# Kernel tuning notes

Measured on AMD Instinct MI355X. Metric: run time of the kernel, lower is better.

The kernel has to match this reference:

```python
import jax, jax.numpy as jnp
import numpy as np

B, S, H = 2, 2048, 4096
NH, NKV, HD = 32, 8, 128
ROPE_THETA = 10000.0


def _rope_tables(seq_len, head_dim, theta):
    inv_freq = 1.0 / (theta ** (jnp.arange(0, head_dim, 2, dtype=jnp.float32) / head_dim))
    t = jnp.arange(seq_len, dtype=jnp.float32)
    freqs = jnp.outer(t, inv_freq)            # [S, HD/2]
    emb = jnp.concatenate([freqs, freqs], axis=-1)  # [S, HD]
    return jnp.cos(emb), jnp.sin(emb)


def _rotate_half(x):
    x1, x2 = jnp.split(x, 2, axis=-1)
    return jnp.concatenate([-x2, x1], axis=-1)


def setup_inputs() -> dict:
    key = jax.random.key(0)
    ks = jax.random.split(key, 5)
    hidden_states = jax.random.normal(ks[0], (B, S, H), dtype=jnp.float32)
    # causal additive mask [B,1,S,S]
    neg = jnp.finfo(jnp.float32).min
    causal = jnp.where(jnp.tril(jnp.ones((S, S), dtype=bool)), 0.0, neg)
    attention_mask = jnp.broadcast_to(causal[None, None], (B, 1, S, S)).astype(jnp.float32)
    position_ids = jnp.broadcast_to(jnp.arange(S, dtype=jnp.int64)[None], (B, S))
    scale = 0.02
    Wq = jax.random.normal(ks[1], (H, H), dtype=jnp.float32) * scale
    Wk = jax.random.normal(ks[2], (NKV * HD, H), dtype=jnp.float32) * scale
    Wv = jax.random.normal(ks[3], (NKV * HD, H), dtype=jnp.float32) * scale
    Wo = jax.random.normal(ks[4], (H, H), dtype=jnp.float32) * scale
    return {"hidden_states": hidden_states, "attention_mask": attention_mask,
            "position_ids": position_ids, "Wq": Wq, "Wk": Wk, "Wv": Wv, "Wo": Wo}


def reference(hidden_states, attention_mask, position_ids, Wq, Wk, Wv, Wo):
    bsz, q_len, _ = hidden_states.shape
    # projections (nn.Linear: x @ W.T)
    q = (hidden_states @ Wq.T).reshape(bsz, q_len, NH, HD).transpose(0, 2, 1, 3)    # [B,NH,S,HD]
    k = (hidden_states @ Wk.T).reshape(bsz, q_len, NKV, HD).transpose(0, 2, 1, 3)   # [B,NKV,S,HD]
    v = (hidden_states @ Wv.T).reshape(bsz, q_len, NKV, HD).transpose(0, 2, 1, 3)
    # RoPE
    cos, sin = _rope_tables(q_len, HD, ROPE_THETA)
    cos = cos[position_ids][:, None]   # [B,1,S,HD]
    sin = sin[position_ids][:, None]
    q = q * cos + _rotate_half(q) * sin
    k = k * cos + _rotate_half(k) * sin
    # repeat_kv (GQA): [B,NKV,S,HD] -> [B,NH,S,HD]
    n_rep = NH // NKV
    k = jnp.repeat(k, n_rep, axis=1)
    v = jnp.repeat(v, n_rep, axis=1)
    # attention
    attn = jnp.einsum('bhqd,bhkd->bhqk', q, k) / jnp.sqrt(jnp.float32(HD))
    attn = attn + attention_mask
    attn = jax.nn.softmax(attn.astype(jnp.float32), axis=-1).astype(q.dtype)
    out = jnp.einsum('bhqk,bhkd->bhqd', attn, v)           # [B,NH,S,HD]
    out = out.transpose(0, 2, 1, 3).reshape(bsz, q_len, NH * HD)
    return out @ Wo.T
```

## Files before the change

### kernel.cpp

```cpp
#include <hip/hip_runtime.h>
#include <hip/hip_bf16.h>


typedef __bf16 bf16;
typedef __bf16 bf16x8 __attribute__((ext_vector_type(8)));
typedef float f32x4 __attribute__((ext_vector_type(4)));

#define UNROLL _Pragma("unroll")

__device__ __forceinline__ void async16(const bf16* g, bf16* l) {
  __builtin_amdgcn_global_load_lds(
      (const __attribute__((address_space(1))) void*)g,
      (__attribute__((address_space(3))) void*)l,
      16, 0, 0);
}

#define BARR { __builtin_amdgcn_s_barrier(); }
#define VMCNT(n) { asm volatile("s_waitcnt vmcnt(" #n ")" ::: "memory"); }

__global__ void k_cvt(const float* __restrict__ s, bf16* __restrict__ d, int n8) {
  int i = blockIdx.x * 256 + threadIdx.x;
  if (i >= n8) return;
  const float4* sp = (const float4*)s + (size_t)i * 2;
  float4 a = sp[0], b = sp[1];
  bf16x8 o = { (bf16)a.x, (bf16)a.y, (bf16)a.z, (bf16)a.w,
               (bf16)b.x, (bf16)b.y, (bf16)b.z, (bf16)b.w };
  *(bf16x8*)(d + (size_t)i * 8) = o;
}

__global__ void k_cvt4(const float* __restrict__ Xs, const float* __restrict__ Wq,
                       const float* __restrict__ Wk, const float* __restrict__ Wv,
                       bf16* __restrict__ Xb, bf16* __restrict__ Wqkv) {
  int u = blockIdx.x * 256 + threadIdx.x;
  const float* sp;
  bf16* dp;
  size_t off;
  if (u < 2097152) { sp = Xs; dp = Xb; off = u; }
  else if (u < 4194304) { sp = Wq; dp = Wqkv; off = u - 2097152; }
  else if (u < 4718592) { sp = Wk; dp = Wqkv + 16777216u; off = u - 4194304; }
  else { sp = Wv; dp = Wqkv + 20971520u; off = u - 4718592; }
  const float4* s4 = (const float4*)sp + off * 2;
  float4 a = s4[0], b = s4[1];
  bf16x8 o = { (bf16)a.x, (bf16)a.y, (bf16)a.z, (bf16)a.w,
               (bf16)b.x, (bf16)b.y, (bf16)b.z, (bf16)b.w };
  *(bf16x8*)(dp + off * 8) = o;
}

template <typename OutT, int SPLIT>
__global__ __launch_bounds__(512, 2) void k_gemmCS(
    const bf16* __restrict__ A, const bf16* __restrict__ Bw,
    OutT* __restrict__ C, int lda, int Kloop, int ldc, int nbx, size_t csplit) {
  __shared__ __align__(16) bf16 lds[2][4][8192];
  const int tid = threadIdx.x;
  const int lane = tid & 63;
  const int w = tid >> 6;
  const int wm = w >> 2, wn = w & 3;
  const int l16 = lane & 15, lh = lane >> 4;

  const int cpx = gridDim.x >> 3;
  const int swz = (blockIdx.x & 7) * cpx + (blockIdx.x >> 3);
  int by, bx;
  if (SPLIT) {
    const int kh = swz >> 7;
    const int t = swz & 127;
    by = t >> 3;
    bx = t & 7;
    A += (size_t)kh * 2048;
    Bw += (size_t)kh * 2048;
    C += (size_t)kh * csplit;
  } else {
    by = swz / nbx;
    bx = swz % nbx;
  }
  const size_t m0 = (size_t)by * 256, n0 = (size_t)bx * 256;

  const int row0 = tid >> 2;
  const int cOff = ((tid & 3) ^ ((row0 >> 1) & 3)) * 8;
  const bf16* pA0 = A + (m0 + row0) * lda + cOff;
  const bf16* pA1 = pA0 + (size_t)128 * lda;
  const bf16* pB0 = Bw + (n0 + row0) * lda + cOff;
  const bf16* pB1 = pB0 + (size_t)128 * lda;

#define SA(s, h, t)                                        \
  { const int kk = (t) * 64 + (h) * 32;                    \
    async16(pA0 + kk, &lds[s][h][0] + tid * 8);            \
    async16(pA1 + kk, &lds[s][h][0] + 4096 + tid * 8); }
#define SB(s, h, t)                                        \
  { const int kk = (t) * 64 + (h) * 32;                    \
    async16(pB0 + kk, &lds[s][2 + (h)][0] + tid * 8);      \
    async16(pB1 + kk, &lds[s][2 + (h)][0] + 4096 + tid * 8); }

#define RDA(s, u, mh)                                                 \
  UNROLL for (int x = 0; x < 4; ++x) {                                \
    int p = (wm * 128 + (mh) * 64 + x * 16 + l16) * 64 + lh * 16;     \
    p ^= ((p >> 7) & 3) << 4;                                         \
    Ar[x] = *(const bf16x8*)((const char*)&lds[s][u][0] + p);         \
  }
#define RDB(s, u)                                                     \
  UNROLL for (int y = 0; y < 4; ++y) {                                \
    int p = (wn * 64 + y * 16 + l16) * 64 + lh * 16;                  \
    p ^= ((p >> 7) & 3) << 4;                                         \
    Br[y] = *(const bf16x8*)((const char*)&lds[s][u][0] + p);         \
  }
#define MF(mh)                                                        \
  { __builtin_amdgcn_s_setprio(1);                                    \
    UNROLL for (int x = 0; x < 4; ++x)                                \
      UNROLL for (int y = 0; y < 4; ++y)                              \
        acc[(mh) * 4 + x][y] = __builtin_amdgcn_mfma_f32_16x16x32_bf16( \
            Ar[x], Br[y], acc[(mh) * 4 + x][y], 0, 0, 0);             \
    __builtin_amdgcn_s_setprio(0); }

  f32x4 acc[8][4] = {};
  const int NITER = Kloop >> 7;

  SA(0, 0, 0); SB(0, 0, 0); SA(0, 1, 0); SB(0, 1, 0); SA(1, 0, 1); SB(1, 0, 1);
  VMCNT(8);

#define ITER_BODY(i, LAST)                                                  \
  { const int t0 = 2 * (i), t1 = t0 + 1;                                    \
    bf16x8 Ar[4], Br[4];                                                    \
    BARR; RDA(0, 0, 0); RDB(0, 2); SA(1, 1, t1); MF(0);                     \
    BARR; RDA(0, 0, 1); SB(1, 1, t1); MF(1); VMCNT(8);                      \
    BARR; RDA(0, 1, 0); RDB(0, 3); if (!(LAST)) SA(0, 0, t0 + 2); MF(0);    \
    BARR; RDA(0, 1, 1); if (!(LAST)) SB(0, 0, t0 + 2); MF(1);               \
    if (LAST) { VMCNT(4); } else { VMCNT(8); }                              \
    BARR; RDA(1, 0, 0); RDB(1, 2); if (!(LAST)) SA(0, 1, t0 + 2); MF(0);    \
    BARR; RDA(1, 0, 1); if (!(LAST)) SB(0, 1, t0 + 2); MF(1);               \
    if (LAST) { VMCNT(0); } else { VMCNT(8); }                              \
    BARR; RDA(1, 1, 0); RDB(1, 3); if (!(LAST)) SA(1, 0, t1 + 2); MF(0);    \
    BARR; RDA(1, 1, 1); if (!(LAST)) SB(1, 0, t1 + 2); MF(1);               \
    if (!(LAST)) VMCNT(8); }

  for (int i = 0; i < NITER - 1; ++i) ITER_BODY(i, 0);
  ITER_BODY(NITER - 1, 1);

  UNROLL for (int mi = 0; mi < 8; ++mi) {
    size_t row = m0 + wm * 128 + mi * 16 + lh * 4;
    UNROLL for (int ni = 0; ni < 4; ++ni) {
      size_t col = n0 + wn * 64 + ni * 16 + l16;
      UNROLL for (int j = 0; j < 4; ++j)
        C[(row + j) * ldc + col] = (OutT)acc[mi][ni][j];
    }
  }
#undef SA
#undef SB
#undef RDA
#undef RDB
#undef MF
#undef ITER_BODY
}

__global__ void k_rope(const bf16* __restrict__ QKV, const bf16* __restrict__ Sp,
                       bf16* __restrict__ Qr, bf16* __restrict__ Kr) {
  int gid = blockIdx.x * 256 + threadIdx.x;
  int seg = gid & 7;
  int rest = gid >> 3;
  int slot = rest % 40;
  int tok = rest / 40;
  int s = tok & 2047;
  int b = tok >> 11;
  float x1v[8], x2v[8];
  if (slot < 32) {
    const bf16* src = QKV + (size_t)tok * 6144 + slot * 128 + seg * 8;
    bf16x8 a = *(const bf16x8*)src;
    bf16x8 c = *(const bf16x8*)(src + 64);
    UNROLL for (int j = 0; j < 8; ++j) { x1v[j] = (float)a[j]; x2v[j] = (float)c[j]; }
  } else {
    const bf16* src = Sp + (size_t)tok * 2048 + (slot - 32) * 128 + seg * 8;
    bf16x8 a0 = *(const bf16x8*)src;
    bf16x8 a1 = *(const bf16x8*)(src + 8388608);
    bf16x8 c0 = *(const bf16x8*)(src + 64);
    bf16x8 c1 = *(const bf16x8*)(src + 8388608 + 64);
    UNROLL for (int j = 0; j < 8; ++j) {
      x1v[j] = (float)a0[j] + (float)a1[j];
      x2v[j] = (float)c0[j] + (float)c1[j];
    }
  }
  bf16x8 o1v, o2v;
  const float scale = (slot < 32) ? 0.08838834764831845f : 1.0f;
  UNROLL for (int j = 0; j < 8; ++j) {
    int p = seg * 8 + j;
    float f = exp2f((float)p * (-13.287712379549449f / 64.0f));
    float sn, cn;
    sincosf((float)s * f, &sn, &cn);
    o1v[j] = (bf16)((x1v[j] * cn - x2v[j] * sn) * scale);
    o2v[j] = (bf16)((x2v[j] * cn + x1v[j] * sn) * scale);
  }
  bf16* dst;
  if (slot < 32) {
    dst = Qr + (((size_t)b * 32 + slot) * 2048 + s) * 128 + seg * 8;
  } else {
    dst = Kr + (((size_t)b * 8 + (slot - 32)) * 2048 + s) * 128 + seg * 8;
  }
  *(bf16x8*)dst = o1v;
  *(bf16x8*)(dst + 64) = o2v;
}

__global__ void k_vtrans(const bf16* __restrict__ Sp, bf16* __restrict__ Vtg) {
  __shared__ __align__(16) bf16 T[64 * 64];
  const int tid = threadIdx.x;
  const int dt = blockIdx.x & 1;
  const int st = (blockIdx.x >> 1) & 31;
  const int hh = blockIdx.x >> 6;
  const int hkv = hh & 7, b = hh >> 3;
  const int s0 = st * 64, d0 = dt * 64;
  const bf16* src = Sp + (size_t)(b * 2048 + s0) * 2048 + 1024 + hkv * 128 + d0;
  UNROLL for (int k = 0; k < 2; ++k) {
    int cc = tid * 2 + k;
    int r = cc >> 3, c8 = cc & 7;
    const bf16* p0 = src + (size_t)r * 2048 + c8 * 8;
    bf16x8 a0 = *(const bf16x8*)p0;
    bf16x8 a1 = *(const bf16x8*)(p0 + 8388608);
    bf16x8 v;
    UNROLL for (int j = 0; j < 8; ++j) v[j] = (bf16)((float)a0[j] + (float)a1[j]);
    int byte = (r * 128 + c8 * 16) ^ ((r & 7) << 4);
    *(bf16x8*)((char*)T + byte) = v;
  }
  __syncthreads();
  bf16* dst = Vtg + ((size_t)(b * 8 + hkv) * 128 + d0) * 2048 + s0;
  UNROLL for (int k = 0; k < 2; ++k) {
    int cc = tid * 2 + k;
    int d = cc >> 3, s8 = cc & 7;
    bf16x8 v;
    UNROLL for (int j = 0; j < 8; ++j) {
      int s = s8 * 8 + j;
      int byte = (s * 128 + d * 2) ^ ((s & 7) << 4);
      v[j] = *(const bf16*)((const char*)T + byte);
    }
    *(bf16x8*)(dst + (size_t)d * 2048 + s8 * 8) = v;
  }
}

__global__ __launch_bounds__(256, 2) void k_flash(
    const bf16* __restrict__ Qr, const bf16* __restrict__ Kr,
    const bf16* __restrict__ Vtg, bf16* __restrict__ Out) {
  __shared__ __align__(16) bf16 Kl[2][64 * 128];
  __shared__ __align__(16) bf16 Vl[2][128 * 64];
  __shared__ __align__(16) bf16 Pl[4][32 * 64];
  const int tid = threadIdx.x;
  const int lane = tid & 63;
  const int w = tid >> 6;
  const int l16 = lane & 15, lh = lane >> 4;
  const int bid = blockIdx.x;
  const int stream = ((bid >> 8) << 3) | (bid & 7);
  const int inner = (bid >> 3) & 31;
  const int b = stream >> 3;
  const int hkv = stream & 7;
  const int h = hkv * 4 + (inner >> 3);
  const int pid = inner & 7;
  const bf16* Kbase = Kr + ((size_t)stream) * 2048 * 128;
  const bf16* Vbase = Vtg + ((size_t)stream) * 128 * 2048;
  bf16* P = &Pl[w][0];

  int kOff[4], vOff[4], ldsOff[4];
  UNROLL for (int i = 0; i < 4; ++i) {
    int c = (w * 4 + i) * 64 + lane;
    ldsOff[i] = c * 8;
    int r = c >> 4, p = c & 15;
    kOff[i] = r * 128 + (p ^ (r & 7)) * 8;
    int r2 = c >> 3, p2 = c & 7;
    vOff[i] = r2 * 2048 + (p2 ^ (r2 & 7)) * 8;
  }

  bf16x8 ones;
  UNROLL for (int j = 0; j < 8; ++j) ones[j] = (bf16)1.0f;

  for (int qi = 0; qi < 2; ++qi) {
    const int q = qi ? (15 - pid) : pid;
    const int q0 = q * 128;
    const int nt = 2 * q + 2;

    bf16x8 qf[2][4];
    UNROLL for (int m = 0; m < 2; ++m) {
      const bf16* qb = Qr + (((size_t)(b * 32 + h)) * 2048 + q0 + w * 32 + m * 16 + l16) * 128 + lh * 8;
      UNROLL for (int kc = 0; kc < 4; ++kc) qf[m][kc] = *(const bf16x8*)(qb + kc * 32);
    }
    f32x4 acc[2][8] = {};
    f32x4 accS[2] = {};
    float mrow[2][4] = {{-1e30f, -1e30f, -1e30f, -1e30f}, {-1e30f, -1e30f, -1e30f, -1e30f}};

    UNROLL for (int i = 0; i < 4; ++i) {
      async16(Kbase + kOff[i], &Kl[0][0] + ldsOff[i]);
      async16(Vbase + vOff[i], &Vl[0][0] + ldsOff[i]);
    }
    __syncthreads();

    for (int t = 0; t < nt; ++t) {
      const int cur = t & 1;
      if (t + 1 < nt) {
        const int nb = t + 1;
        UNROLL for (int i = 0; i < 4; ++i) {
          async16(Kbase + (size_t)nb * 8192 + kOff[i], &Kl[cur ^ 1][0] + ldsOff[i]);
          async16(Vbase + (size_t)nb * 64 + vOff[i], &Vl[cur ^ 1][0] + ldsOff[i]);
        }
      }
      f32x4 sf[2][4] = {};
      __builtin_amdgcn_s_setprio(1);
      UNROLL for (int ni = 0; ni < 4; ++ni) {
        int row = ni * 16 + l16;
        bf16x8 kf[4];
        UNROLL for (int kc = 0; kc < 4; ++kc) {
          int byte = (row * 256 + kc * 64 + lh * 16) ^ ((row & 7) << 4);
          kf[kc] = *(const bf16x8*)((const char*)&Kl[cur][0] + byte);
        }
        UNROLL for (int m = 0; m < 2; ++m)
          UNROLL for (int kc = 0; kc < 4; ++kc)
            sf[m][ni] = __builtin_amdgcn_mfma_f32_16x16x32_bf16(qf[m][kc], kf[kc], sf[m][ni], 0, 0, 0);
      }
      __builtin_amdgcn_s_setprio(0);
      if (t >= 2 * q) {
        UNROLL for (int m = 0; m < 2; ++m)
          UNROLL for (int ni = 0; ni < 4; ++ni) {
            int key = t * 64 + ni * 16 + l16;
            UNROLL for (int j = 0; j < 4; ++j) {
              int rowg = q0 + w * 32 + m * 16 + lh * 4 + j;
              if (key > rowg) sf[m][ni][j] = -1e30f;
            }
          }
      }
      float corr[2][4];
      UNROLL for (int m = 0; m < 2; ++m)
        UNROLL for (int j = 0; j < 4; ++j) {
          float mx = fmaxf(fmaxf(sf[m][0][j], sf[m][1][j]), fmaxf(sf[m][2][j], sf[m][3][j]));
          mx = fmaxf(mx, __shfl_xor(mx, 1));
          mx = fmaxf(mx, __shfl_xor(mx, 2));
          mx = fmaxf(mx, __shfl_xor(mx, 4));
          mx = fmaxf(mx, __shfl_xor(mx, 8));
          float mn = fmaxf(mrow[m][j], mx);
          corr[m][j] = __expf(mrow[m][j] - mn);
          mrow[m][j] = mn;
          UNROLL for (int ni = 0; ni < 4; ++ni)
            sf[m][ni][j] = __expf(sf[m][ni][j] - mn);
        }
      UNROLL for (int m = 0; m < 2; ++m) {
        UNROLL for (int di = 0; di < 8; ++di)
          UNROLL for (int j = 0; j < 4; ++j) acc[m][di][j] *= corr[m][j];
        UNROLL for (int j = 0; j < 4; ++j) accS[m][j] *= corr[m][j];
      }
      UNROLL for (int m = 0; m < 2; ++m)
        UNROLL for (int ni = 0; ni < 4; ++ni)
          UNROLL for (int j = 0; j < 4; ++j) {
            int row = m * 16 + lh * 4 + j;
            int byte = (row * 128 + ni * 32 + l16 * 2) ^ ((row & 7) << 4);
            *(bf16*)((char*)P + byte) = (bf16)sf[m][ni][j];
          }
      UNROLL for (int kc = 0; kc < 2; ++kc) {
        bf16x8 pa[2];
        UNROLL for (int m = 0; m < 2; ++m) {
          int row = m * 16 + l16;
          int byte = (row * 128 + kc * 64 + lh * 16) ^ ((row & 7) << 4);
          pa[m] = *(const bf16x8*)((const char*)P + byte);
        }
        __builtin_amdgcn_s_setprio(1);
        UNROLL for (int m = 0; m < 2; ++m)
          accS[m] = __builtin_amdgcn_mfma_f32_16x16x32_bf16(pa[m], ones, accS[m], 0, 0, 0);
        UNROLL for (int di = 0; di < 8; ++di) {
          int d = di * 16 + l16;
          int byte = (d * 128 + kc * 64 + lh * 16) ^ ((d & 7) << 4);
          bf16x8 vb = *(const bf16x8*)((const char*)&Vl[cur][0] + byte);
          UNROLL for (int m = 0; m < 2; ++m)
            acc[m][di] = __builtin_amdgcn_mfma_f32_16x16x32_bf16(pa[m], vb, acc[m][di], 0, 0, 0);
        }
        __builtin_amdgcn_s_setprio(0);
      }
      __syncthreads();
    }

    UNROLL for (int m = 0; m < 2; ++m)
      UNROLL for (int j = 0; j < 4; ++j) {
        float inv = 1.0f / accS[m][j];
        int rowg = q0 + w * 32 + m * 16 + lh * 4 + j;
        bf16* ob = Out + ((size_t)(b * 2048) + rowg) * 4096 + h * 128 + l16;
        UNROLL for (int di = 0; di < 8; ++di)
          ob[di * 16] = (bf16)(acc[m][di][j] * inv);
      }
  }
}

extern "C" void kernel_launch(void* const* d_in, const int* in_sizes, int n_in,
                              void* d_out, int out_size, void* d_ws, size_t ws_size,
                              hipStream_t stream) {
  const float* hidden = (const float*)d_in[0];
  const float* Wq = (const float*)d_in[3];
  const float* Wk = (const float*)d_in[4];
  const float* Wv = (const float*)d_in[5];
  const float* Wo = (const float*)d_in[6];
  float* out = (float*)d_out;

  char* ws = (char*)d_ws;
  if (ws_size < 184549376u) return;
  bf16* Xb = (bf16*)(ws);
  bf16* Wqkv = (bf16*)(ws + 33554432u);
  bf16* QKV = (bf16*)(ws + 83886080u);
  bf16* Qr = (bf16*)(ws + 134217728u);
  bf16* Kr = (bf16*)(ws + 167772160u);
  bf16* Vtg = (bf16*)(ws + 176160768u);
  bf16* AttnO = Xb;
  bf16* Wob = Wqkv;
  bf16* Spart = Wqkv;

  k_cvt4<<<20480, 256, 0, stream>>>(hidden, Wq, Wk, Wv, Xb, Wqkv);
  k_gemmCS<bf16, 0><<<256, 512, 0, stream>>>(Xb, Wqkv, QKV, 4096, 4096, 6144, 16, 0);
  k_gemmCS<bf16, 1><<<256, 512, 0, stream>>>(
      Xb, Wqkv + (size_t)4096 * 4096, Spart, 4096, 2048, 2048, 8, 8388608u);
  k_rope<<<5120, 256, 0, stream>>>(QKV, Spart, Qr, Kr);
  k_vtrans<<<1024, 256, 0, stream>>>(Spart, Vtg);
  k_cvt<<<8192, 256, 0, stream>>>(Wo, Wob, 2097152);
  k_flash<<<512, 256, 0, stream>>>(Qr, Kr, Vtg, AttnO);
  k_gemmCS<float, 0><<<256, 512, 0, stream>>>(AttnO, Wob, out, 4096, 4096, 4096, 16, 0);
}
```

Measured before the change: 525.4 us.

## Fuse Q RoPE into flash attention, merge prep kernels, add lazy softmax rescale

Q rotary embedding and scaling move into the flash kernel's Q fragment load, reading directly from the packed QKV buffer, so the separate Qr intermediate is no longer written and re-read. K RoPE, V transpose and the Wo bf16 conversion are merged into one k_prep launch, with Wob given its own workspace slot to avoid aliasing with Spart. The online softmax skips the accumulator rescale when the tile max grows by at most 8 over the running max, trading fewer multiplies for exponentials bounded by e^8 in bf16 P.

```diff
diff --git a/kernel.cpp b/kernel.cpp
--- a/kernel.cpp
+++ b/kernel.cpp
@@ -17,16 +17,6 @@
 
 #define BARR { __builtin_amdgcn_s_barrier(); }
 #define VMCNT(n) { asm volatile("s_waitcnt vmcnt(" #n ")" ::: "memory"); }
-
-__global__ void k_cvt(const float* __restrict__ s, bf16* __restrict__ d, int n8) {
-  int i = blockIdx.x * 256 + threadIdx.x;
-  if (i >= n8) return;
-  const float4* sp = (const float4*)s + (size_t)i * 2;
-  float4 a = sp[0], b = sp[1];
-  bf16x8 o = { (bf16)a.x, (bf16)a.y, (bf16)a.z, (bf16)a.w,
-               (bf16)b.x, (bf16)b.y, (bf16)b.z, (bf16)b.w };
-  *(bf16x8*)(d + (size_t)i * 8) = o;
-}
 
 __global__ void k_cvt4(const float* __restrict__ Xs, const float* __restrict__ Wq,
                        const float* __restrict__ Wk, const float* __restrict__ Wv,
@@ -150,89 +140,83 @@
 #undef ITER_BODY
 }
 
-__global__ void k_rope(const bf16* __restrict__ QKV, const bf16* __restrict__ Sp,
-                       bf16* __restrict__ Qr, bf16* __restrict__ Kr) {
-  int gid = blockIdx.x * 256 + threadIdx.x;
-  int seg = gid & 7;
-  int rest = gid >> 3;
-  int slot = rest % 40;
-  int tok = rest / 40;
-  int s = tok & 2047;
-  int b = tok >> 11;
-  float x1v[8], x2v[8];
-  if (slot < 32) {
-    const bf16* src = QKV + (size_t)tok * 6144 + slot * 128 + seg * 8;
-    bf16x8 a = *(const bf16x8*)src;
-    bf16x8 c = *(const bf16x8*)(src + 64);
-    UNROLL for (int j = 0; j < 8; ++j) { x1v[j] = (float)a[j]; x2v[j] = (float)c[j]; }
-  } else {
-    const bf16* src = Sp + (size_t)tok * 2048 + (slot - 32) * 128 + seg * 8;
+__global__ void k_prep(const float* __restrict__ Wo, const bf16* __restrict__ Sp,
+                       bf16* __restrict__ Kr, bf16* __restrict__ Vtg,
+                       bf16* __restrict__ Wob) {
+  __shared__ __align__(16) bf16 T[64 * 64];
+  const int bid = blockIdx.x;
+  const int tid = threadIdx.x;
+  if (bid < 1024) {
+    int gid = bid * 256 + tid;
+    int seg = gid & 7;
+    int rest = gid >> 3;
+    int slot8 = rest & 7;
+    int tok = rest >> 3;
+    int s = tok & 2047;
+    int b = tok >> 11;
+    const bf16* src = Sp + (size_t)tok * 2048 + slot8 * 128 + seg * 8;
     bf16x8 a0 = *(const bf16x8*)src;
     bf16x8 a1 = *(const bf16x8*)(src + 8388608);
     bf16x8 c0 = *(const bf16x8*)(src + 64);
     bf16x8 c1 = *(const bf16x8*)(src + 8388608 + 64);
+    bf16x8 o1v, o2v;
     UNROLL for (int j = 0; j < 8; ++j) {
-      x1v[j] = (float)a0[j] + (float)a1[j];
-      x2v[j] = (float)c0[j] + (float)c1[j];
-    }
-  }
-  bf16x8 o1v, o2v;
-  const float scale = (slot < 32) ? 0.08838834764831845f : 1.0f;
-  UNROLL for (int j = 0; j < 8; ++j) {
-    int p = seg * 8 + j;
-    float f = exp2f((float)p * (-13.287712379549449f / 64.0f));
-    float sn, cn;
-    sincosf((float)s * f, &sn, &cn);
-    o1v[j] = (bf16)((x1v[j] * cn - x2v[j] * sn) * scale);
-    o2v[j] = (bf16)((x2v[j] * cn + x1v[j] * sn) * scale);
-  }
-  bf16* dst;
-  if (slot < 32) {
-    dst = Qr + (((size_t)b * 32 + slot) * 2048 + s) * 128 + seg * 8;
+      float x1 = (float)a0[j] + (float)a1[j];
+      float x2 = (float)c0[j] + (float)c1[j];
+      int p = seg * 8 + j;
+      float f = exp2f((float)p * (-13.287712379549449f / 64.0f));
+      float sn, cn;
+      sincosf((float)s * f, &sn, &cn);
+      o1v[j] = (bf16)(x1 * cn - x2 * sn);
+      o2v[j] = (bf16)(x2 * cn + x1 * sn);
+    }
+    bf16* dst = Kr + (((size_t)b * 8 + slot8) * 2048 + s) * 128 + seg * 8;
+    *(bf16x8*)dst = o1v;
+    *(bf16x8*)(dst + 64) = o2v;
+  } else if (bid < 2048) {
+    const int vb = bid - 1024;
+    const int dt = vb & 1;
+    const int st = (vb >> 1) & 31;
+    const int hh = vb >> 6;
+    const int hkv = hh & 7, b = hh >> 3;
+    const int s0 = st * 64, d0 = dt * 64;
+    const bf16* src = Sp + (size_t)(b * 2048 + s0) * 2048 + 1024 + hkv * 128 + d0;
+    UNROLL for (int k = 0; k < 2; ++k) {
+      int cc = tid * 2 + k;
+      int r = cc >> 3, c8 = cc & 7;
+      const bf16* p0 = src + (size_t)r * 2048 + c8 * 8;
+      bf16x8 a0 = *(const bf16x8*)p0;
+      bf16x8 a1 = *(const bf16x8*)(p0 + 8388608);
+      bf16x8 v;
+      UNROLL for (int j = 0; j < 8; ++j) v[j] = (bf16)((float)a0[j] + (float)a1[j]);
+      int byte = (r * 128 + c8 * 16) ^ ((r & 7) << 4);
+      *(bf16x8*)((char*)T + byte) = v;
+    }
+    __syncthreads();
+    bf16* dst = Vtg + ((size_t)(b * 8 + hkv) * 128 + d0) * 2048 + s0;
+    UNROLL for (int k = 0; k < 2; ++k) {
+      int cc = tid * 2 + k;
+      int d = cc >> 3, s8 = cc & 7;
+      bf16x8 v;
+      UNROLL for (int j = 0; j < 8; ++j) {
+        int s = s8 * 8 + j;
+        int byte = (s * 128 + d * 2) ^ ((s & 7) << 4);
+        v[j] = *(const bf16*)((const char*)T + byte);
+      }
+      *(bf16x8*)(dst + (size_t)d * 2048 + s8 * 8) = v;
+    }
   } else {
-    dst = Kr + (((size_t)b * 8 + (slot - 32)) * 2048 + s) * 128 + seg * 8;
-  }
-  *(bf16x8*)dst = o1v;
-  *(bf16x8*)(dst + 64) = o2v;
-}
-
-__global__ void k_vtrans(const bf16* __restrict__ Sp, bf16* __restrict__ Vtg) {
-  __shared__ __align__(16) bf16 T[64 * 64];
-  const int tid = threadIdx.x;
-  const int dt = blockIdx.x & 1;
-  const int st = (blockIdx.x >> 1) & 31;
-  const int hh = blockIdx.x >> 6;
-  const int hkv = hh & 7, b = hh >> 3;
-  const int s0 = st * 64, d0 = dt * 64;
-  const bf16* src = Sp + (size_t)(b * 2048 + s0) * 2048 + 1024 + hkv * 128 + d0;
-  UNROLL for (int k = 0; k < 2; ++k) {
-    int cc = tid * 2 + k;
-    int r = cc >> 3, c8 = cc & 7;
-    const bf16* p0 = src + (size_t)r * 2048 + c8 * 8;
-    bf16x8 a0 = *(const bf16x8*)p0;
-    bf16x8 a1 = *(const bf16x8*)(p0 + 8388608);
-    bf16x8 v;
-    UNROLL for (int j = 0; j < 8; ++j) v[j] = (bf16)((float)a0[j] + (float)a1[j]);
-    int byte = (r * 128 + c8 * 16) ^ ((r & 7) << 4);
-    *(bf16x8*)((char*)T + byte) = v;
-  }
-  __syncthreads();
-  bf16* dst = Vtg + ((size_t)(b * 8 + hkv) * 128 + d0) * 2048 + s0;
-  UNROLL for (int k = 0; k < 2; ++k) {
-    int cc = tid * 2 + k;
-    int d = cc >> 3, s8 = cc & 7;
-    bf16x8 v;
-    UNROLL for (int j = 0; j < 8; ++j) {
-      int s = s8 * 8 + j;
-      int byte = (s * 128 + d * 2) ^ ((s & 7) << 4);
-      v[j] = *(const bf16*)((const char*)T + byte);
-    }
-    *(bf16x8*)(dst + (size_t)d * 2048 + s8 * 8) = v;
+    int i = (bid - 2048) * 256 + tid;
+    const float4* s4 = (const float4*)Wo + (size_t)i * 2;
+    float4 a = s4[0], b = s4[1];
+    bf16x8 o = { (bf16)a.x, (bf16)a.y, (bf16)a.z, (bf16)a.w,
+                 (bf16)b.x, (bf16)b.y, (bf16)b.z, (bf16)b.w };
+    *(bf16x8*)(Wob + (size_t)i * 8) = o;
   }
 }
 
 __global__ __launch_bounds__(256, 2) void k_flash(
-    const bf16* __restrict__ Qr, const bf16* __restrict__ Kr,
+    const bf16* __restrict__ QKV, const bf16* __restrict__ Kr,
     const bf16* __restrict__ Vtg, bf16* __restrict__ Out) {
   __shared__ __align__(16) bf16 Kl[2][64 * 128];
   __shared__ __align__(16) bf16 Vl[2][128 * 64];
@@ -272,9 +256,21 @@
 
     bf16x8 qf[2][4];
     UNROLL for (int m = 0; m < 2; ++m) {
-      const bf16* qb = Qr + (((size_t)(b * 32 + h)) * 2048 + q0 + w * 32 + m * 16 + l16) * 128 + lh * 8;
+      const int srow = q0 + w * 32 + m * 16 + l16;
+      const bf16* qb = QKV + (size_t)(b * 2048 + srow) * 6144 + h * 128 + lh * 8;
       UNROLL for (int kc = 0; kc < 4; ++kc) qf[m][kc] = *(const bf16x8*)(qb + kc * 32);
-    }
+      UNROLL for (int kc = 0; kc < 2; ++kc)
+        UNROLL for (int j = 0; j < 8; ++j) {
+          int d = lh * 8 + kc * 32 + j;
+          float f = exp2f((float)d * (-13.287712379549449f / 64.0f));
+          float sn, cn;
+          sincosf((float)srow * f, &sn, &cn);
+          float x1 = (float)qf[m][kc][j], x2 = (float)qf[m][kc + 2][j];
+          qf[m][kc][j] = (bf16)((x1 * cn - x2 * sn) * 0.08838834764831845f);
+          qf[m][kc + 2][j] = (bf16)((x2 * cn + x1 * sn) * 0.08838834764831845f);
+        }
+    }
+
     f32x4 acc[2][8] = {};
     f32x4 accS[2] = {};
     float mrow[2][4] = {{-1e30f, -1e30f, -1e30f, -1e30f}, {-1e30f, -1e30f, -1e30f, -1e30f}};
@@ -318,25 +314,36 @@
             }
           }
       }
-      float corr[2][4];
+      float mx[2][4];
+      bool dfr = true;
       UNROLL for (int m = 0; m < 2; ++m)
         UNROLL for (int j = 0; j < 4; ++j) {
-          float mx = fmaxf(fmaxf(sf[m][0][j], sf[m][1][j]), fmaxf(sf[m][2][j], sf[m][3][j]));
-          mx = fmaxf(mx, __shfl_xor(mx, 1));
-          mx = fmaxf(mx, __shfl_xor(mx, 2));
-          mx = fmaxf(mx, __shfl_xor(mx, 4));
-          mx = fmaxf(mx, __shfl_xor(mx, 8));
-          float mn = fmaxf(mrow[m][j], mx);
-          corr[m][j] = __expf(mrow[m][j] - mn);
-          mrow[m][j] = mn;
-          UNROLL for (int ni = 0; ni < 4; ++ni)
-            sf[m][ni][j] = __expf(sf[m][ni][j] - mn);
-        }
-      UNROLL for (int m = 0; m < 2; ++m) {
-        UNROLL for (int di = 0; di < 8; ++di)
-          UNROLL for (int j = 0; j < 4; ++j) acc[m][di][j] *= corr[m][j];
-        UNROLL for (int j = 0; j < 4; ++j) accS[m][j] *= corr[m][j];
-      }
+          float v = fmaxf(fmaxf(sf[m][0][j], sf[m][1][j]), fmaxf(sf[m][2][j], sf[m][3][j]));
+          v = fmaxf(v, __shfl_xor(v, 1));
+          v = fmaxf(v, __shfl_xor(v, 2));
+          v = fmaxf(v, __shfl_xor(v, 4));
+          v = fmaxf(v, __shfl_xor(v, 8));
+          mx[m][j] = v;
+          dfr = dfr && (v <= mrow[m][j] + 8.0f);
+        }
+      if (!__all(dfr)) {
+        float corr[2][4];
+        UNROLL for (int m = 0; m < 2; ++m)
+          UNROLL for (int j = 0; j < 4; ++j) {
+            float mn = fmaxf(mrow[m][j], mx[m][j]);
+            corr[m][j] = __expf(mrow[m][j] - mn);
+            mrow[m][j] = mn;
+          }
+        UNROLL for (int m = 0; m < 2; ++m) {
+          UNROLL for (int di = 0; di < 8; ++di)
+            UNROLL for (int j = 0; j < 4; ++j) acc[m][di][j] *= corr[m][j];
+          UNROLL for (int j = 0; j < 4; ++j) accS[m][j] *= corr[m][j];
+        }
+      }
+      UNROLL for (int m = 0; m < 2; ++m)
+        UNROLL for (int ni = 0; ni < 4; ++ni)
+          UNROLL for (int j = 0; j < 4; ++j)
+            sf[m][ni][j] = __expf(sf[m][ni][j] - mrow[m][j]);
       UNROLL for (int m = 0; m < 2; ++m)
         UNROLL for (int ni = 0; ni < 4; ++ni)
           UNROLL for (int j = 0; j < 4; ++j) {
@@ -392,20 +399,17 @@
   bf16* Xb = (bf16*)(ws);
   bf16* Wqkv = (bf16*)(ws + 33554432u);
   bf16* QKV = (bf16*)(ws + 83886080u);
-  bf16* Qr = (bf16*)(ws + 134217728u);
+  bf16* Wob = (bf16*)(ws + 134217728u);
   bf16* Kr = (bf16*)(ws + 167772160u);
   bf16* Vtg = (bf16*)(ws + 176160768u);
   bf16* AttnO = Xb;
-  bf16* Wob = Wqkv;
   bf16* Spart = Wqkv;
 
   k_cvt4<<<20480, 256, 0, stream>>>(hidden, Wq, Wk, Wv, Xb, Wqkv);
   k_gemmCS<bf16, 0><<<256, 512, 0, stream>>>(Xb, Wqkv, QKV, 4096, 4096, 6144, 16, 0);
   k_gemmCS<bf16, 1><<<256, 512, 0, stream>>>(
       Xb, Wqkv + (size_t)4096 * 4096, Spart, 4096, 2048, 2048, 8, 8388608u);
-  k_rope<<<5120, 256, 0, stream>>>(QKV, Spart, Qr, Kr);
-  k_vtrans<<<1024, 256, 0, stream>>>(Spart, Vtg);
-  k_cvt<<<8192, 256, 0, stream>>>(Wo, Wob, 2097152);
-  k_flash<<<512, 256, 0, stream>>>(Qr, Kr, Vtg, AttnO);
+  k_prep<<<10240, 256, 0, stream>>>(Wo, Spart, Kr, Vtg, Wob);
+  k_flash<<<512, 256, 0, stream>>>(QKV, Kr, Vtg, AttnO);
   k_gemmCS<float, 0><<<256, 512, 0, stream>>>(AttnO, Wob, out, 4096, 4096, 4096, 16, 0);
 }
```

New measurement: 514.9 us. -2.0%, faster.
